# Kernel optimization log

Measured on AMD Instinct MI355X. Metric: run time of the kernel, lower is better.

The kernel has to match this reference:

```python
import jax, jax.numpy as jnp
import numpy as np

N = 200_000   # nodes
E = 6_400_000 # edges (avg degree 32)


def setup_inputs() -> dict:
    key = jax.random.key(0)
    k = jax.random.split(key, 6)
    x = jax.random.normal(k[0], (N, 2), dtype=jnp.float32)
    edge_index = jax.random.randint(k[1], (2, E), 0, N, dtype=jnp.int32)
    # GCNConv(2, 8) and GCNConv(8, 4) parameters (Glorot-ish init, zero bias as in PyG)
    W1 = jax.random.normal(k[2], (2, 8), dtype=jnp.float32) * (1.0 / np.sqrt(2.0))
    b1 = jnp.zeros((8,), dtype=jnp.float32)
    W2 = jax.random.normal(k[3], (8, 4), dtype=jnp.float32) * (1.0 / np.sqrt(8.0))
    b2 = jnp.zeros((4,), dtype=jnp.float32)
    return {"x": x, "edge_index": edge_index, "W1": W1, "b1": b1, "W2": W2, "b2": b2}


def _gcn_conv(x, src, dst, norm, W, b, n):
    # PyG GCNConv: linear transform, normalized gather/scatter-add, bias after aggregation
    h = x @ W                                   # [N, F_out]
    msg = h[src] * norm[:, None]                # gather + edge-wise scale, [E', F_out]
    agg = jax.ops.segment_sum(msg, dst, num_segments=n)  # scatter-add at targets
    return agg + b


def reference(x, edge_index, W1, b1, W2, b2):
    n = x.shape[0]
    # add self-loops (PyG default add_self_loops=True)
    loops = jnp.arange(n, dtype=edge_index.dtype)
    src = jnp.concatenate([edge_index[0], loops])
    dst = jnp.concatenate([edge_index[1], loops])
    # symmetric degree normalization: deg computed at targets with unit edge weights
    deg = jax.ops.segment_sum(jnp.ones_like(src, dtype=x.dtype), dst, num_segments=n)
    deg_inv_sqrt = jnp.where(deg > 0, jax.lax.rsqrt(jnp.maximum(deg, 1.0)), 0.0)
    norm = deg_inv_sqrt[src] * deg_inv_sqrt[dst]  # [E']

    h = jax.nn.relu(_gcn_conv(x, src, dst, norm, W1, b1, n))
    out = _gcn_conv(h, src, dst, norm, W2, b2, n)
    return out
```

## Files before the change

kernel.cpp:

```cpp
#include <hip/hip_runtime.h>


#define EPB   8192
#define PART  2048
#define LPBIT 11
#define SRCB  18
#define BC    4
#define RSTR  2049
#define STCAP 17408
#define NSL1  256
#define CAP1  2304
#define NSL2  128
#define CAP2  1280


__global__ __launch_bounds__(512) void countA_kernel(
    const int* __restrict__ dst, int* __restrict__ cntmat, int E, int P) {
    __shared__ int cnt[128];
    int tid = threadIdx.x;
    if (tid < 128) cnt[tid] = 0;
    __syncthreads();
    int nv4 = E >> 2;
    int b4 = (blockIdx.x * EPB) >> 2;
    int e4 = min(b4 + (EPB >> 2), nv4);
    const int4* d4 = (const int4*)dst;
    #pragma unroll
    for (int k = 0; k < (EPB >> 2); k += 512) {
        int i = b4 + k + tid;
        if (i < e4) {
            int4 d = d4[i];
            atomicAdd(&cnt[d.x >> LPBIT], 1);
            atomicAdd(&cnt[d.y >> LPBIT], 1);
            atomicAdd(&cnt[d.z >> LPBIT], 1);
            atomicAdd(&cnt[d.w >> LPBIT], 1);
        }
    }
    if (blockIdx.x == gridDim.x - 1) {
        int e = (nv4 << 2) + tid;
        if (e < E) atomicAdd(&cnt[dst[e] >> LPBIT], 1);
    }
    __syncthreads();
    int* row = cntmat + (size_t)blockIdx.x * P;
    if (tid < P) row[tid] = cnt[tid];
}

__global__ __launch_bounds__(256) void colscanA_kernel(
    int* __restrict__ cntmat, int* __restrict__ colTotal, int B, int P) {
    __shared__ int sdata[256];
    int p = blockIdx.x, tid = threadIdx.x;
    int v[4];
    int s = 0;
    #pragma unroll
    for (int k = 0; k < 4; k++) {
        int b = tid * 4 + k;
        v[k] = (b < B) ? cntmat[(size_t)b * P + p] : 0;
        s += v[k];
    }
    int x = s;
    sdata[tid] = x;
    __syncthreads();
    for (int off = 1; off < 256; off <<= 1) {
        int t = (tid >= off) ? sdata[tid - off] : 0;
        __syncthreads();
        x += t;
        sdata[tid] = x;
        __syncthreads();
    }
    int run = x - s;
    #pragma unroll
    for (int k = 0; k < 4; k++) {
        int b = tid * 4 + k;
        if (b < B) cntmat[(size_t)b * P + p] = run;
        run += v[k];
    }
    if (tid == 255) colTotal[p] = x;
}

__global__ __launch_bounds__(256) void totalscanA_kernel(
    const int* __restrict__ colTotal, int* __restrict__ colStart,
    int P, int E) {
    __shared__ int sdata[256];
    int tid = threadIdx.x;
    int v[4];
    int s = 0;
    #pragma unroll
    for (int k = 0; k < 4; k++) {
        int i = tid * 4 + k;
        v[k] = (i < P) ? colTotal[i] : 0;
        s += v[k];
    }
    int x = s;
    sdata[tid] = x;
    __syncthreads();
    for (int off = 1; off < 256; off <<= 1) {
        int t = (tid >= off) ? sdata[tid - off] : 0;
        __syncthreads();
        x += t;
        sdata[tid] = x;
        __syncthreads();
    }
    int run = x - s;
    #pragma unroll
    for (int k = 0; k < 4; k++) {
        int i = tid * 4 + k;
        if (i < P) colStart[i] = run;
        run += v[k];
    }
    if (tid == 0) colStart[P] = E;
}

__global__ __launch_bounds__(512) void scatterA_kernel(
    const int* __restrict__ src, const int* __restrict__ dst,
    const int* __restrict__ cntmat, const int* __restrict__ colStart,
    unsigned* __restrict__ packed, int E, int P) {
    __shared__ int cur[128];
    int tid = threadIdx.x;
    if (tid < P) cur[tid] = colStart[tid] + cntmat[(size_t)blockIdx.x * P + tid];
    __syncthreads();
    int nv4 = E >> 2;
    int b4 = (blockIdx.x * EPB) >> 2;
    int e4 = min(b4 + (EPB >> 2), nv4);
    const int4* d4 = (const int4*)dst;
    const int4* s4 = (const int4*)src;
    #pragma unroll
    for (int k = 0; k < (EPB >> 2); k += 512) {
        int i = b4 + k + tid;
        if (i < e4) {
            int4 d = d4[i];
            int4 sv = s4[i];
            int p0 = atomicAdd(&cur[d.x >> LPBIT], 1);
            packed[p0] = ((unsigned)(d.x & (PART - 1)) << SRCB) | (unsigned)sv.x;
            int p1 = atomicAdd(&cur[d.y >> LPBIT], 1);
            packed[p1] = ((unsigned)(d.y & (PART - 1)) << SRCB) | (unsigned)sv.y;
            int p2 = atomicAdd(&cur[d.z >> LPBIT], 1);
            packed[p2] = ((unsigned)(d.z & (PART - 1)) << SRCB) | (unsigned)sv.z;
            int p3 = atomicAdd(&cur[d.w >> LPBIT], 1);
            packed[p3] = ((unsigned)(d.w & (PART - 1)) << SRCB) | (unsigned)sv.w;
        }
    }
    if (blockIdx.x == gridDim.x - 1) {
        int e = (nv4 << 2) + tid;
        if (e < E) {
            int d = dst[e];
            int pos = atomicAdd(&cur[d >> LPBIT], 1);
            packed[pos] = ((unsigned)(d & (PART - 1)) << SRCB) | (unsigned)src[e];
        }
    }
}


__global__ __launch_bounds__(512) void localC_kernel(
    const unsigned* __restrict__ packed, const int* __restrict__ colStart,
    int* __restrict__ runStart, int* __restrict__ srcsorted) {
    __shared__ int hist[PART];
    __shared__ int sdata[512];
    __shared__ unsigned stage[STCAP];
    int tid = threadIdx.x;
    int dp = blockIdx.x >> 2, b = blockIdx.x & (BC - 1);
    int s0 = colStart[dp], len = colStart[dp + 1] - s0;
    int lo = s0 + (int)(((long long)len * b) / BC);
    int hi = s0 + (int)(((long long)len * (b + 1)) / BC);
    for (int k = tid; k < PART; k += 512) hist[k] = 0;
    __syncthreads();
    for (int i = lo + tid; i < hi; i += 512)
        atomicAdd(&hist[packed[i] >> SRCB], 1);
    __syncthreads();
    int off = tid * 4;
    int v0 = hist[off], v1 = hist[off + 1], v2 = hist[off + 2], v3 = hist[off + 3];
    int s = v0 + v1 + v2 + v3;
    int x = s;
    sdata[tid] = x;
    __syncthreads();
    for (int o = 1; o < 512; o <<= 1) {
        int t = (tid >= o) ? sdata[tid - o] : 0;
        __syncthreads();
        x += t;
        sdata[tid] = x;
        __syncthreads();
    }
    int run = x - s;
    int* rs = runStart + (size_t)(dp * BC + b) * RSTR;
    int c0 = lo + run, c1 = c0 + v0, c2 = c1 + v1, c3 = c2 + v2;
    rs[off] = c0; rs[off + 1] = c1; rs[off + 2] = c2; rs[off + 3] = c3;
    __syncthreads();
    hist[off] = c0; hist[off + 1] = c1; hist[off + 2] = c2; hist[off + 3] = c3;
    if (tid == 0) rs[PART] = hi;
    __syncthreads();
    int total = hi - lo;
    bool ovf = total > STCAP;
    for (int i = lo + tid; i < hi; i += 512) {
        unsigned w = packed[i];
        int pos = atomicAdd(&hist[w >> SRCB], 1);
        unsigned sv = w & ((1u << SRCB) - 1);
        if (!ovf) stage[pos - lo] = sv;
        else srcsorted[pos] = (int)sv;
    }
    __syncthreads();
    if (!ovf)
        for (int j = tid; j < total; j += 512) srcsorted[lo + j] = (int)stage[j];
}


__global__ __launch_bounds__(512) void dinvg_kernel(
    const int* __restrict__ runStart, const float* __restrict__ x,
    float* __restrict__ dinv, float* __restrict__ g, int n) {
    int i = blockIdx.x * 512 + threadIdx.x;
    if (i >= n) return;
    int dp = i >> LPBIT, ld = i & (PART - 1);
    int deg = 0;
    #pragma unroll
    for (int b = 0; b < BC; b++) {
        const int* rs = runStart + (size_t)(dp * BC + b) * RSTR + ld;
        deg += rs[1] - rs[0];
    }
    float d = rsqrtf((float)deg + 1.0f);
    dinv[i] = d;
    float2 xv = ((const float2*)x)[i];
    ((float2*)g)[i] = make_float2(xv.x * d, xv.y * d);
}


__global__ __launch_bounds__(512) void agg1f_kernel(
    const int* __restrict__ srcsorted, const int* __restrict__ runStart,
    const float* __restrict__ g, const float* __restrict__ dinv,
    const float* __restrict__ W1, const float* __restrict__ b1,
    const float* __restrict__ W2, float* __restrict__ hs2, int n) {
    __shared__ float2 stage[CAP1];
    __shared__ int srs[NSL1 + 1];
    __shared__ float sres[NSL1][2];
    int tid = threadIdx.x;
    int dp = blockIdx.x >> 3, sl = blockIdx.x & 7;
    int nid = tid >> 1, c = tid & 1;
    const float2* gp = (const float2*)g;
    float acc = 0.0f;
    #pragma unroll
    for (int b = 0; b < BC; b++) {
        const int* rs = runStart + (size_t)(dp * BC + b) * RSTR + sl * NSL1;
        if (tid <= NSL1) srs[tid] = rs[tid];
        __syncthreads();
        int lo = srs[0], hi = srs[NSL1];
        bool ovf = (hi - lo) > CAP1;
        if (!ovf)
            for (int e = lo + tid; e < hi; e += 512)
                stage[e - lo] = gp[srcsorted[e]];
        __syncthreads();
        int a = srs[nid] - lo, bnd = srs[nid + 1] - lo;
        if (!ovf) {
            const float* st = (const float*)stage;
            for (int j = a; j < bnd; j++) acc += st[j * 2 + c];
        } else {
            for (int j = a; j < bnd; j++)
                acc += g[2 * (size_t)srcsorted[lo + j] + c];
        }
        __syncthreads();
    }
    sres[nid][c] = acc;
    __syncthreads();
    if (tid < NSL1) {
        int i = ((dp << LPBIT) | (sl * NSL1)) + tid;
        if (i < n) {
            float d = dinv[i];
            float2 gi = gp[i];
            float s0 = (sres[tid][0] + gi.x) * d;
            float s1 = (sres[tid][1] + gi.y) * d;
            float oc0 = 0.0f, oc1 = 0.0f, oc2 = 0.0f, oc3 = 0.0f;
            #pragma unroll
            for (int f = 0; f < 8; f++) {
                float h = fmaxf(s0 * W1[f] + s1 * W1[8 + f] + b1[f], 0.0f);
                oc0 += h * W2[4 * f];
                oc1 += h * W2[4 * f + 1];
                oc2 += h * W2[4 * f + 2];
                oc3 += h * W2[4 * f + 3];
            }
            float4 o;
            o.x = oc0 * d; o.y = oc1 * d; o.z = oc2 * d; o.w = oc3 * d;
            ((float4*)hs2)[i] = o;
        }
    }
}

__global__ __launch_bounds__(512) void agg2f_kernel(
    const int* __restrict__ srcsorted, const int* __restrict__ runStart,
    const float* __restrict__ hs2, const float* __restrict__ dinv,
    const float* __restrict__ b2, float* __restrict__ out, int n) {
    __shared__ float4 stage[CAP2];
    __shared__ int srs[NSL2 + 1];
    int tid = threadIdx.x;
    int dp = blockIdx.x >> 4, sl = blockIdx.x & 15;
    int nid = tid >> 2, c = tid & 3;
    const float4* hp = (const float4*)hs2;
    float acc = 0.0f;
    #pragma unroll
    for (int b = 0; b < BC; b++) {
        const int* rs = runStart + (size_t)(dp * BC + b) * RSTR + sl * NSL2;
        if (tid <= NSL2) srs[tid] = rs[tid];
        __syncthreads();
        int lo = srs[0], hi = srs[NSL2];
        bool ovf = (hi - lo) > CAP2;
        if (!ovf)
            for (int e = lo + tid; e < hi; e += 512)
                stage[e - lo] = hp[srcsorted[e]];
        __syncthreads();
        int a = srs[nid] - lo, bnd = srs[nid + 1] - lo;
        if (!ovf) {
            const float* st = (const float*)stage;
            for (int j = a; j < bnd; j++) acc += st[j * 4 + c];
        } else {
            for (int j = a; j < bnd; j++)
                acc += hs2[4 * (size_t)srcsorted[lo + j] + c];
        }
        __syncthreads();
    }
    int i = ((dp << LPBIT) | (sl * NSL2)) + nid;
    if (i < n) {
        float d = dinv[i];
        float hv = hs2[4 * (size_t)i + c];
        out[4 * (size_t)i + c] = d * (acc + hv) + b2[c];
    }
}

extern "C" void kernel_launch(void* const* d_in, const int* in_sizes, int n_in,
                              void* d_out, int out_size, void* d_ws, size_t ws_size,
                              hipStream_t stream) {
    const float* x   = (const float*)d_in[0];
    const int*   ei  = (const int*)d_in[1];
    const float* W1  = (const float*)d_in[2];
    const float* b1  = (const float*)d_in[3];
    const float* W2  = (const float*)d_in[4];
    const float* b2  = (const float*)d_in[5];
    float* out = (float*)d_out;

    const int n = in_sizes[0] / 2;
    const int E = in_sizes[1] / 2;
    const int* src = ei;
    const int* dst = ei + E;

    const int P  = (n + PART - 1) >> LPBIT;
    const int B1 = (E + EPB - 1) / EPB;

    int* ws = (int*)d_ws;
    int* colTotal = ws;
    int* colStart = ws + 1024;
    int* cntmatA  = ws + 2048;
    size_t cmsz = (((size_t)B1 * P) + 3) & ~(size_t)3;
    int* runStart = cntmatA + cmsz;
    size_t rssz = (((size_t)P * BC * RSTR) + 3) & ~(size_t)3;
    unsigned* packed = (unsigned*)(runStart + rssz);
    int* srcsorted = (int*)(packed + E);
    size_t nd = (size_t)P << LPBIT;
    float* dinv = (float*)packed;
    float* g    = dinv + nd;
    float* hs2  = g + 2 * nd;

    const int gN  = (n + 511) / 512;
    const int gA1 = P * (PART / NSL1);
    const int gA2 = P * (PART / NSL2);

    countA_kernel    <<<B1, 512, 0, stream>>>(dst, cntmatA, E, P);
    colscanA_kernel  <<<P, 256, 0, stream>>>(cntmatA, colTotal, B1, P);
    totalscanA_kernel<<<1, 256, 0, stream>>>(colTotal, colStart, P, E);
    scatterA_kernel  <<<B1, 512, 0, stream>>>(src, dst, cntmatA, colStart, packed, E, P);
    localC_kernel    <<<P * BC, 512, 0, stream>>>(packed, colStart, runStart, srcsorted);
    dinvg_kernel     <<<gN, 512, 0, stream>>>(runStart, x, dinv, g, n);
    agg1f_kernel     <<<gA1, 512, 0, stream>>>(srcsorted, runStart, g, dinv, W1, b1, W2, hs2, n);
    agg2f_kernel     <<<gA2, 512, 0, stream>>>(srcsorted, runStart, hs2, dinv, b2, out, n);
}
```

Baseline: 235.0 us.

## Stage all bucket gathers at once in aggregation kernels with smaller node slices

Both aggregation kernels now load the run-start offsets and gather source features for all four buckets into shared memory in one phase behind a single barrier. Previously they looped over buckets with three barriers each. Each block now covers half as many nodes, and pairs of threads split the buckets for each node, combining their partial sums through shared memory. The aim is more memory-level parallelism in the gathers and fewer barrier stalls. The costs are more blocks, an extra reduction step, and per-bucket staging capacities that are smaller in absolute terms, so the slow overflow path may be taken more often.

Result: slower. 248.0 us (+5.5%).

```diff
diff --git a/kernel.cpp b/kernel.cpp
--- a/kernel.cpp
+++ b/kernel.cpp
@@ -8,10 +8,10 @@
 #define BC    4
 #define RSTR  2049
 #define STCAP 17408
-#define NSL1  256
-#define CAP1  2304
-#define NSL2  128
-#define CAP2  1280
+#define NSL1  128
+#define CAP1B 1200
+#define NSL2  64
+#define CAP2B 640
 
 
 __global__ __launch_bounds__(512) void countA_kernel(
@@ -220,57 +220,65 @@
 }
 
 
-__global__ __launch_bounds__(512) void agg1f_kernel(
+__global__ __launch_bounds__(512) void agg1g_kernel(
     const int* __restrict__ srcsorted, const int* __restrict__ runStart,
     const float* __restrict__ g, const float* __restrict__ dinv,
     const float* __restrict__ W1, const float* __restrict__ b1,
     const float* __restrict__ W2, float* __restrict__ hs2, int n) {
-    __shared__ float2 stage[CAP1];
-    __shared__ int srs[NSL1 + 1];
-    __shared__ float sres[NSL1][2];
-    int tid = threadIdx.x;
-    int dp = blockIdx.x >> 3, sl = blockIdx.x & 7;
-    int nid = tid >> 1, c = tid & 1;
+    __shared__ float2 stage[BC][CAP1B];
+    __shared__ int srs[BC][NSL1 + 1];
+    __shared__ float sres[NSL1][2][2];
+    int tid = threadIdx.x;
+    int dp = blockIdx.x >> 4, sl = blockIdx.x & 15;
+    for (int k = tid; k < BC * (NSL1 + 1); k += 512) {
+        int b = k / (NSL1 + 1), idx = k - b * (NSL1 + 1);
+        srs[b][idx] = runStart[(size_t)(dp * BC + b) * RSTR + sl * NSL1 + idx];
+    }
+    __syncthreads();
     const float2* gp = (const float2*)g;
+    int lo[BC];
+    bool ovf[BC];
+    #pragma unroll
+    for (int b = 0; b < BC; b++) {
+        lo[b] = srs[b][0];
+        int hi = srs[b][NSL1];
+        ovf[b] = (hi - lo[b]) > CAP1B;
+        if (!ovf[b])
+            for (int e = lo[b] + tid; e < hi; e += 512)
+                stage[b][e - lo[b]] = gp[srcsorted[e]];
+    }
+    __syncthreads();
+    int c = tid & 1, h = (tid >> 1) & 1, nid = tid >> 2;
     float acc = 0.0f;
     #pragma unroll
-    for (int b = 0; b < BC; b++) {
-        const int* rs = runStart + (size_t)(dp * BC + b) * RSTR + sl * NSL1;
-        if (tid <= NSL1) srs[tid] = rs[tid];
-        __syncthreads();
-        int lo = srs[0], hi = srs[NSL1];
-        bool ovf = (hi - lo) > CAP1;
-        if (!ovf)
-            for (int e = lo + tid; e < hi; e += 512)
-                stage[e - lo] = gp[srcsorted[e]];
-        __syncthreads();
-        int a = srs[nid] - lo, bnd = srs[nid + 1] - lo;
-        if (!ovf) {
-            const float* st = (const float*)stage;
+    for (int bb = 0; bb < 2; bb++) {
+        int b = h * 2 + bb;
+        int a = srs[b][nid] - lo[b], bnd = srs[b][nid + 1] - lo[b];
+        if (!ovf[b]) {
+            const float* st = (const float*)&stage[b][0];
             for (int j = a; j < bnd; j++) acc += st[j * 2 + c];
         } else {
             for (int j = a; j < bnd; j++)
-                acc += g[2 * (size_t)srcsorted[lo + j] + c];
-        }
-        __syncthreads();
-    }
-    sres[nid][c] = acc;
+                acc += g[2 * (size_t)srcsorted[lo[b] + j] + c];
+        }
+    }
+    sres[nid][c][h] = acc;
     __syncthreads();
     if (tid < NSL1) {
         int i = ((dp << LPBIT) | (sl * NSL1)) + tid;
         if (i < n) {
             float d = dinv[i];
             float2 gi = gp[i];
-            float s0 = (sres[tid][0] + gi.x) * d;
-            float s1 = (sres[tid][1] + gi.y) * d;
+            float s0 = (sres[tid][0][0] + sres[tid][0][1] + gi.x) * d;
+            float s1 = (sres[tid][1][0] + sres[tid][1][1] + gi.y) * d;
             float oc0 = 0.0f, oc1 = 0.0f, oc2 = 0.0f, oc3 = 0.0f;
             #pragma unroll
             for (int f = 0; f < 8; f++) {
-                float h = fmaxf(s0 * W1[f] + s1 * W1[8 + f] + b1[f], 0.0f);
-                oc0 += h * W2[4 * f];
-                oc1 += h * W2[4 * f + 1];
-                oc2 += h * W2[4 * f + 2];
-                oc3 += h * W2[4 * f + 3];
+                float h2 = fmaxf(s0 * W1[f] + s1 * W1[8 + f] + b1[f], 0.0f);
+                oc0 += h2 * W2[4 * f];
+                oc1 += h2 * W2[4 * f + 1];
+                oc2 += h2 * W2[4 * f + 2];
+                oc3 += h2 * W2[4 * f + 3];
             }
             float4 o;
             o.x = oc0 * d; o.y = oc1 * d; o.z = oc2 * d; o.w = oc3 * d;
@@ -279,43 +287,58 @@
     }
 }
 
-__global__ __launch_bounds__(512) void agg2f_kernel(
+__global__ __launch_bounds__(512) void agg2g_kernel(
     const int* __restrict__ srcsorted, const int* __restrict__ runStart,
     const float* __restrict__ hs2, const float* __restrict__ dinv,
     const float* __restrict__ b2, float* __restrict__ out, int n) {
-    __shared__ float4 stage[CAP2];
-    __shared__ int srs[NSL2 + 1];
-    int tid = threadIdx.x;
-    int dp = blockIdx.x >> 4, sl = blockIdx.x & 15;
-    int nid = tid >> 2, c = tid & 3;
+    __shared__ float4 stage[BC][CAP2B];
+    __shared__ int srs[BC][NSL2 + 1];
+    __shared__ float sres[NSL2][4][2];
+    int tid = threadIdx.x;
+    int dp = blockIdx.x >> 5, sl = blockIdx.x & 31;
+    for (int k = tid; k < BC * (NSL2 + 1); k += 512) {
+        int b = k / (NSL2 + 1), idx = k - b * (NSL2 + 1);
+        srs[b][idx] = runStart[(size_t)(dp * BC + b) * RSTR + sl * NSL2 + idx];
+    }
+    __syncthreads();
     const float4* hp = (const float4*)hs2;
+    int lo[BC];
+    bool ovf[BC];
+    #pragma unroll
+    for (int b = 0; b < BC; b++) {
+        lo[b] = srs[b][0];
+        int hi = srs[b][NSL2];
+        ovf[b] = (hi - lo[b]) > CAP2B;
+        if (!ovf[b])
+            for (int e = lo[b] + tid; e < hi; e += 512)
+                stage[b][e - lo[b]] = hp[srcsorted[e]];
+    }
+    __syncthreads();
+    int c = tid & 3, h = (tid >> 2) & 1, nid = tid >> 3;
     float acc = 0.0f;
     #pragma unroll
-    for (int b = 0; b < BC; b++) {
-        const int* rs = runStart + (size_t)(dp * BC + b) * RSTR + sl * NSL2;
-        if (tid <= NSL2) srs[tid] = rs[tid];
-        __syncthreads();
-        int lo = srs[0], hi = srs[NSL2];
-        bool ovf = (hi - lo) > CAP2;
-        if (!ovf)
-            for (int e = lo + tid; e < hi; e += 512)
-                stage[e - lo] = hp[srcsorted[e]];
-        __syncthreads();
-        int a = srs[nid] - lo, bnd = srs[nid + 1] - lo;
-        if (!ovf) {
-            const float* st = (const float*)stage;
+    for (int bb = 0; bb < 2; bb++) {
+        int b = h * 2 + bb;
+        int a = srs[b][nid] - lo[b], bnd = srs[b][nid + 1] - lo[b];
+        if (!ovf[b]) {
+            const float* st = (const float*)&stage[b][0];
             for (int j = a; j < bnd; j++) acc += st[j * 4 + c];
         } else {
             for (int j = a; j < bnd; j++)
-                acc += hs2[4 * (size_t)srcsorted[lo + j] + c];
-        }
-        __syncthreads();
-    }
-    int i = ((dp << LPBIT) | (sl * NSL2)) + nid;
-    if (i < n) {
-        float d = dinv[i];
-        float hv = hs2[4 * (size_t)i + c];
-        out[4 * (size_t)i + c] = d * (acc + hv) + b2[c];
+                acc += hs2[4 * (size_t)srcsorted[lo[b] + j] + c];
+        }
+    }
+    sres[nid][c][h] = acc;
+    __syncthreads();
+    if (tid < NSL2 * 4) {
+        int nid2 = tid >> 2, c2 = tid & 3;
+        int i = ((dp << LPBIT) | (sl * NSL2)) + nid2;
+        if (i < n) {
+            float d = dinv[i];
+            float hv = hs2[4 * (size_t)i + c2];
+            out[4 * (size_t)i + c2] =
+                d * (sres[nid2][c2][0] + sres[nid2][c2][1] + hv) + b2[c2];
+        }
     }
 }
 
@@ -362,6 +385,6 @@
     scatterA_kernel  <<<B1, 512, 0, stream>>>(src, dst, cntmatA, colStart, packed, E, P);
     localC_kernel    <<<P * BC, 512, 0, stream>>>(packed, colStart, runStart, srcsorted);
     dinvg_kernel     <<<gN, 512, 0, stream>>>(runStart, x, dinv, g, n);
-    agg1f_kernel     <<<gA1, 512, 0, stream>>>(srcsorted, runStart, g, dinv, W1, b1, W2, hs2, n);
-    agg2f_kernel     <<<gA2, 512, 0, stream>>>(srcsorted, runStart, hs2, dinv, b2, out, n);
-}
+    agg1g_kernel     <<<gA1, 512, 0, stream>>>(srcsorted, runStart, g, dinv, W1, b1, W2, hs2, n);
+    agg2g_kernel     <<<gA2, 512, 0, stream>>>(srcsorted, runStart, hs2, dinv, b2, out, n);
+}
```
